# Kernel optimization log

Hardware: AMD Instinct MI355X
Metric: run time of the kernel (lower is better)

The kernel has to match this reference:

```python
import jax, jax.numpy as jnp
import numpy as np

N = 20000      # num clique nodes
E = 320000     # num edges
H = 256        # hidden_channels
OUT = 128      # out_channels
T = 3          # num_timesteps
NEG = 0.01     # GAT negative_slope
NA = 60000     # num atoms (unused arg sizing)


def setup_inputs() -> dict:
    key = jax.random.key(0)
    ks = jax.random.split(key, 12)
    s = 1.0 / np.sqrt(H)
    return {
        "x_clique": jax.random.normal(ks[0], (N, H), jnp.float32),
        "W_gat": jax.random.normal(ks[1], (H, H), jnp.float32) * s,
        "att_src": jax.random.normal(ks[2], (H,), jnp.float32) * s,
        "att_dst": jax.random.normal(ks[3], (H,), jnp.float32) * s,
        "gat_bias": jnp.zeros((H,), jnp.float32),
        "W_ih": jax.random.normal(ks[4], (3 * H, H), jnp.float32) * s,
        "W_hh": jax.random.normal(ks[5], (3 * H, H), jnp.float32) * s,
        "b_ih": jnp.zeros((3 * H,), jnp.float32),
        "b_hh": jnp.zeros((3 * H,), jnp.float32),
        "lin_W": jax.random.normal(ks[6], (OUT, H), jnp.float32) * s,
        "lin_b": jnp.zeros((OUT,), jnp.float32),
        "atom2clique_index": jax.random.randint(ks[7], (2, NA), 0, N, jnp.int64),
        "mol_batch": jax.random.randint(ks[8], (NA,), 0, 32, jnp.int64),
        "clique_batch": jax.random.randint(ks[9], (N,), 0, 32, jnp.int64),
        "clique_edge_index": jax.random.randint(ks[10], (2, E), 0, N, jnp.int64),
    }


def _gat_conv(h, W_gat, att_src, att_dst, gat_bias, src, dst):
    # PyG GATConv, heads=1, no self loops. h: [N,H]
    xp = h @ W_gat.T                                   # [N,H]
    a_e = jax.nn.leaky_relu((xp @ att_src)[src] + (xp @ att_dst)[dst], NEG)  # [E]
    # segment softmax over destination nodes
    m = jax.ops.segment_max(a_e, dst, num_segments=N)  # [N] (-inf for empty)
    e = jnp.exp(a_e - m[dst])                          # [E]
    denom = jax.ops.segment_sum(e, dst, num_segments=N)
    coef = e / jnp.maximum(denom[dst], 1e-16)          # [E]
    out = jax.ops.segment_sum(coef[:, None] * xp[src], dst, num_segments=N)
    return out + gat_bias


def _gru_cell(x, h, W_ih, W_hh, b_ih, b_hh):
    gx = x @ W_ih.T + b_ih                             # [N,3H]
    gh = h @ W_hh.T + b_hh                             # [N,3H]
    xr, xz, xn = jnp.split(gx, 3, axis=-1)
    hr, hz, hn = jnp.split(gh, 3, axis=-1)
    r = jax.nn.sigmoid(xr + hr)
    z = jax.nn.sigmoid(xz + hz)
    n = jnp.tanh(xn + r * hn)
    return (1.0 - z) * n + z * h


def reference(x_clique, W_gat, att_src, att_dst, gat_bias, W_ih, W_hh, b_ih, b_hh,
              lin_W, lin_b, atom2clique_index, mol_batch, clique_batch,
              clique_edge_index):
    src = clique_edge_index[0]
    dst = clique_edge_index[1]
    h = x_clique
    for _ in range(T):  # fixed, small timestep count
        m = _gat_conv(h, W_gat, att_src, att_dst, gat_bias, src, dst)
        m = jax.nn.elu(m)  # dropout p=0.0 -> identity
        h = _gru_cell(m, h, W_ih, W_hh, b_ih, b_hh)
    return h @ lin_W.T + lin_b  # [N, OUT]
```

## Files before the change

kernel.cpp:

```cpp
#include <hip/hip_runtime.h>
#include <math.h>

#define NNODES 20000
#define NROWP  20096
#define NEDGES 320000
#define HDIM   256
#define ODIM   128
#define TSTEPS 3
#define KCAT   512

typedef __bf16 bf16x8 __attribute__((ext_vector_type(8)));
typedef __bf16 bf16x4 __attribute__((ext_vector_type(4)));
typedef float  f32x4  __attribute__((ext_vector_type(4)));

#define LOG2E 1.44269504f
__device__ __forceinline__ float fexp2_(float x){ return __builtin_amdgcn_exp2f(x); }
__device__ __forceinline__ float frcp_(float x){ return __builtin_amdgcn_rcpf(x); }
__device__ __forceinline__ float fsig_(float x){ return frcp_(1.f + fexp2_(-LOG2E*x)); }
__device__ __forceinline__ float ftanh_(float x){ float t = fexp2_(2.f*LOG2E*x); return 1.f - 2.f*frcp_(t+1.f); }
__device__ __forceinline__ float felu_(float x){ return (x>0.f)? x : (fexp2_(LOG2E*x)-1.f); }

__device__ __forceinline__ void load_lds16(const void* g, void* l){
  __builtin_amdgcn_global_load_lds((const __attribute__((address_space(1))) void*)g,
                                   (__attribute__((address_space(3))) void*)l, 16, 0, 0);
}

__device__ __forceinline__ bf16x8 lds_frag64(const __bf16* Ls, int rowbase, int lane, int kk){
  int row = rowbase + (lane&15);
  int g = (lane>>4) + (kk<<2);
  int slot = (row<<3) + (g ^ (row&7));
  return *(const bf16x8*)&Ls[slot<<3];
}

__global__ void setup1_kernel(const int* __restrict__ dst, int* __restrict__ deg,
                              const float* __restrict__ xc, __bf16* __restrict__ Acat,
                              const float* __restrict__ Wih, const float* __restrict__ Whh,
                              const float* __restrict__ Wg, const float* __restrict__ Lw,
                              __bf16* __restrict__ Bf, __bf16* __restrict__ wgb,
                              __bf16* __restrict__ lwb, float* __restrict__ asad){
  int i = blockIdx.x*blockDim.x + threadIdx.x;
  if (i < NEDGES) atomicAdd(&deg[dst[i]], 1);
  if (i < NNODES*64){
    int row = i>>6, c = (i&63)<<2;
    float4 v = *(const float4*)&xc[(size_t)row*HDIM + c];
    bf16x4 o; o[0]=(__bf16)v.x; o[1]=(__bf16)v.y; o[2]=(__bf16)v.z; o[3]=(__bf16)v.w;
    *(bf16x4*)&Acat[(size_t)row*KCAT + 256 + c] = o;
  }
  if (i < 1024*128){
    int row = i>>7, kc = (i&127)<<2;
    int gate = row>>8, c = row&255;
    float4 v = make_float4(0,0,0,0);
    if (gate==0 || gate==1){
      v = (kc<256) ? *(const float4*)&Wih[(size_t)(gate*256+c)*HDIM + kc]
                   : *(const float4*)&Whh[(size_t)(gate*256+c)*HDIM + kc-256];
    } else if (gate==2){
      if (kc<256) v = *(const float4*)&Wih[(size_t)(512+c)*HDIM + kc];
    } else {
      if (kc>=256) v = *(const float4*)&Whh[(size_t)(512+c)*HDIM + kc-256];
    }
    bf16x4 o; o[0]=(__bf16)v.x; o[1]=(__bf16)v.y; o[2]=(__bf16)v.z; o[3]=(__bf16)v.w;
    *(bf16x4*)&Bf[(size_t)row*KCAT + kc] = o;
  } else if (i < 1024*128 + 256*64){
    int j = i - 1024*128;
    float4 v = ((const float4*)Wg)[j];
    bf16x4 o; o[0]=(__bf16)v.x; o[1]=(__bf16)v.y; o[2]=(__bf16)v.z; o[3]=(__bf16)v.w;
    ((bf16x4*)wgb)[j] = o;
  } else if (i < 1024*128 + 256*64 + 128*64){
    int j = i - 1024*128 - 256*64;
    float4 v = ((const float4*)Lw)[j];
    bf16x4 o; o[0]=(__bf16)v.x; o[1]=(__bf16)v.y; o[2]=(__bf16)v.z; o[3]=(__bf16)v.w;
    ((bf16x4*)lwb)[j] = o;
  }
  if (i < 2*NNODES) asad[i] = 0.f;
}

__global__ void scan_kernel(const int* __restrict__ deg, int* __restrict__ rowptr){
  const int PER = 20;
  int tid = threadIdx.x, lane = tid&63, w = tid>>6;
  int base = tid*PER;
  int v[PER]; int s = 0;
  #pragma unroll
  for (int k=0;k<PER;k++){
    v[k] = (base+k < NNODES)? deg[base+k] : 0;
    s += v[k];
  }
  int incl = s;
  #pragma unroll
  for (int off=1; off<64; off<<=1){
    int t = __shfl_up(incl, off);
    if (lane >= off) incl += t;
  }
  __shared__ int wtot[16];
  if (lane==63) wtot[w] = incl;
  __syncthreads();
  if (w==0 && lane<16){
    int x = wtot[lane];
    #pragma unroll
    for (int off=1; off<16; off<<=1){
      int t = __shfl_up(x, off);
      if (lane >= off) x += t;
    }
    wtot[lane] = x;
  }
  __syncthreads();
  int wbase = (w>0)? wtot[w-1] : 0;
  int run = wbase + incl - s;
  #pragma unroll
  for (int k=0;k<PER;k++){
    if (base+k < NNODES) rowptr[base+k] = run;
    run += v[k];
  }
  if (tid==1023) rowptr[NNODES] = wbase + incl;
}

__global__ void scatter_kernel(const int* __restrict__ src, const int* __restrict__ dst,
                               const int* __restrict__ rowptr, int* __restrict__ fill,
                               int* __restrict__ ssrc){
  int e = blockIdx.x*blockDim.x + threadIdx.x;
  if (e < NEDGES){
    int d = dst[e];
    int pos = rowptr[d] + atomicAdd(&fill[d], 1);
    ssrc[pos] = src[e];
  }
}

template<int YC, bool F32OUT, bool ALPHA>
__global__ __launch_bounds__(256,4)
void mfma_gemm_sm(const __bf16* __restrict__ A, int lda,
                  const __bf16* __restrict__ B,
                  const float* __restrict__ bias,
                  __bf16* __restrict__ Cb, float* __restrict__ Cf,
                  int ldc, int Mreal,
                  const float* __restrict__ att_s, const float* __restrict__ att_d,
                  float* __restrict__ as_, float* __restrict__ ad_){
  __shared__ __bf16 As[64*64];
  __shared__ __bf16 Bs[128*64];
  int bid = blockIdx.x;
  int r0 = (bid/YC)*64, c0 = (bid%YC)*128;
  int tx = threadIdx.x, lane = tx&63, w = tx>>6;
  int rbase = (w&1)*32, cbase = (w>>1)*64;
  f32x4 acc[2][4] = {};
  for (int k0=0; k0<HDIM; k0+=64){
    #pragma unroll
    for (int q=0;q<2;q++){
      int idx = q*256 + w*64 + lane;
      int row = idx>>3, kg = (idx&7) ^ (row&7);
      load_lds16(A + (size_t)(r0+row)*lda + k0 + (kg<<3),
                 (char*)As + (q*256 + w*64)*16);
    }
    #pragma unroll
    for (int q=0;q<4;q++){
      int idx = q*256 + w*64 + lane;
      int row = idx>>3, kg = (idx&7) ^ (row&7);
      load_lds16(B + (size_t)(c0+row)*HDIM + k0 + (kg<<3),
                 (char*)Bs + (q*256 + w*64)*16);
    }
    __syncthreads();
    #pragma unroll
    for (int kk=0;kk<2;kk++){
      bf16x8 a[2], bb[4];
      #pragma unroll
      for (int i=0;i<2;i++) a[i] = lds_frag64(As, rbase + i*16, lane, kk);
      #pragma unroll
      for (int j=0;j<4;j++) bb[j] = lds_frag64(Bs, cbase + j*16, lane, kk);
      #pragma unroll
      for (int i=0;i<2;i++)
        #pragma unroll
        for (int j=0;j<4;j++)
          acc[i][j] = __builtin_amdgcn_mfma_f32_16x16x32_bf16(a[i], bb[j], acc[i][j], 0,0,0);
    }
    __syncthreads();
  }
  int grb = r0 + rbase, gcb = c0 + cbase;
  #pragma unroll
  for (int i=0;i<2;i++){
    #pragma unroll
    for (int j=0;j<4;j++){
      int gc = gcb + j*16 + (lane&15);
      float bv = F32OUT ? bias[gc] : 0.f;
      #pragma unroll
      for (int r=0;r<4;r++){
        int gr = grb + i*16 + ((lane>>4)<<2) + r;
        if (gr >= Mreal) continue;
        float v = acc[i][j][r] + bv;
        if (F32OUT) Cf[(size_t)gr*ldc + gc] = v;
        else        Cb[(size_t)gr*ldc + gc] = (__bf16)v;
      }
    }
  }
  if (ALPHA){
    float ps[2][4] = {}, pd[2][4] = {};
    #pragma unroll
    for (int j=0;j<4;j++){
      int gc = gcb + j*16 + (lane&15);
      float sv = att_s[gc], dv = att_d[gc];
      #pragma unroll
      for (int i=0;i<2;i++)
        #pragma unroll
        for (int r=0;r<4;r++){
          ps[i][r] += acc[i][j][r]*sv;
          pd[i][r] += acc[i][j][r]*dv;
        }
    }
    #pragma unroll
    for (int m=1;m<16;m<<=1){
      #pragma unroll
      for (int i=0;i<2;i++)
        #pragma unroll
        for (int r=0;r<4;r++){
          ps[i][r] += __shfl_xor(ps[i][r], m);
          pd[i][r] += __shfl_xor(pd[i][r], m);
        }
    }
    if ((lane&15)==0){
      #pragma unroll
      for (int i=0;i<2;i++)
        #pragma unroll
        for (int r=0;r<4;r++){
          int gr = grb + i*16 + ((lane>>4)<<2) + r;
          if (gr < Mreal){
            atomicAdd(&as_[gr], ps[i][r]);
            atomicAdd(&ad_[gr], pd[i][r]);
          }
        }
    }
  }
}

__global__ __launch_bounds__(256,8)
void gat_aggregate_kernel(const __bf16* __restrict__ xpb, const float* __restrict__ as_,
                          const float* __restrict__ ad_, const int* __restrict__ rowptr,
                          const int* __restrict__ ssrc, const float* __restrict__ gat_bias,
                          __bf16* __restrict__ Acat){
  int node = blockIdx.x*4 + (threadIdx.x>>6);
  int lane = threadIdx.x & 63;
  if (node >= NNODES) return;
  int beg = rowptr[node], end = rowptr[node+1];
  int deg = end - beg;
  float adv = ad_[node];
  int half = lane>>5, col = lane&31;

  float acc[8] = {0,0,0,0,0,0,0,0};

  if (deg <= 64){
    float a = -INFINITY; int sreg = 0;
    if (lane < deg){
      sreg = ssrc[beg+lane];
      a = as_[sreg] + adv;
      a = (a>0.f)? a : 0.01f*a;
    }
    float mx = a;
    #pragma unroll
    for (int off=32; off; off>>=1) mx = fmaxf(mx, __shfl_xor(mx,off));
    float e = (lane<deg)? fexp2_(LOG2E*(a-mx)) : 0.f;
    float sm = e;
    #pragma unroll
    for (int off=32; off; off>>=1) sm += __shfl_xor(sm,off);
    float creg = e*frcp_(fmaxf(sm,1e-16f));

    int j = 0;
    for (; j+16<=deg; j+=16){
      float cc[8]; int rr[8]; bf16x8 vv[8];
      #pragma unroll
      for (int k=0;k<8;k++){
        cc[k] = __shfl(creg, j+2*k+half);
        rr[k] = __shfl(sreg, j+2*k+half);
      }
      #pragma unroll
      for (int k=0;k<8;k++) vv[k] = *(const bf16x8*)&xpb[(size_t)rr[k]*HDIM + col*8];
      #pragma unroll
      for (int k=0;k<8;k++)
        #pragma unroll
        for (int t=0;t<8;t++) acc[t] += cc[k]*(float)vv[k][t];
    }
    for (; j+8<=deg; j+=8){
      float cc[4]; int rr[4]; bf16x8 vv[4];
      #pragma unroll
      for (int k=0;k<4;k++){
        cc[k] = __shfl(creg, j+2*k+half);
        rr[k] = __shfl(sreg, j+2*k+half);
      }
      #pragma unroll
      for (int k=0;k<4;k++) vv[k] = *(const bf16x8*)&xpb[(size_t)rr[k]*HDIM + col*8];
      #pragma unroll
      for (int k=0;k<4;k++)
        #pragma unroll
        for (int t=0;t<8;t++) acc[t] += cc[k]*(float)vv[k][t];
    }
    for (; j+4<=deg; j+=4){
      float c0=__shfl(creg,j+half),  c1=__shfl(creg,j+2+half);
      int   r0=__shfl(sreg,j+half),  r1=__shfl(sreg,j+2+half);
      bf16x8 v0 = *(const bf16x8*)&xpb[(size_t)r0*HDIM + col*8];
      bf16x8 v1 = *(const bf16x8*)&xpb[(size_t)r1*HDIM + col*8];
      #pragma unroll
      for (int t=0;t<8;t++) acc[t] += c0*(float)v0[t] + c1*(float)v1[t];
    }
    for (; j<deg; j+=2){
      int jj = j + half;
      float cf = __shfl(creg, jj);
      int   rw = __shfl(sreg, jj);
      if (jj < deg){
        bf16x8 v = *(const bf16x8*)&xpb[(size_t)rw*HDIM + col*8];
        #pragma unroll
        for (int t=0;t<8;t++) acc[t] += cf*(float)v[t];
      }
    }
  } else {
    float mx = -INFINITY;
    for (int e=beg+lane; e<end; e+=64){
      float a = as_[ssrc[e]] + adv;
      a = (a>0.f)? a : 0.01f*a;
      mx = fmaxf(mx, a);
    }
    #pragma unroll
    for (int off=32; off; off>>=1) mx = fmaxf(mx, __shfl_xor(mx,off));
    float sm = 0.f;
    for (int e=beg+lane; e<end; e+=64){
      float a = as_[ssrc[e]] + adv;
      a = (a>0.f)? a : 0.01f*a;
      sm += fexp2_(LOG2E*(a-mx));
    }
    #pragma unroll
    for (int off=32; off; off>>=1) sm += __shfl_xor(sm,off);
    float rsc = frcp_(fmaxf(sm,1e-16f));
    for (int j=0; j<deg; j+=2){
      int jj = j + half;
      if (jj < deg){
        int rw = ssrc[beg+jj];
        float a = as_[rw] + adv;
        a = (a>0.f)? a : 0.01f*a;
        float cf = fexp2_(LOG2E*(a-mx))*rsc;
        bf16x8 v = *(const bf16x8*)&xpb[(size_t)rw*HDIM + col*8];
        #pragma unroll
        for (int t=0;t<8;t++) acc[t] += cf*(float)v[t];
      }
    }
  }

  #pragma unroll
  for (int t=0;t<8;t++) acc[t] += __shfl_down(acc[t], 32);
  if (half==0){
    float4 b0 = *(const float4*)&gat_bias[col*8];
    float4 b1 = *(const float4*)&gat_bias[col*8+4];
    float bb[8] = {b0.x,b0.y,b0.z,b0.w,b1.x,b1.y,b1.z,b1.w};
    bf16x8 ov;
    #pragma unroll
    for (int t=0;t<8;t++) ov[t] = (__bf16)felu_(acc[t]+bb[t]);
    *(bf16x8*)&Acat[(size_t)node*KCAT + col*8] = ov;
  }
}

__global__ __launch_bounds__(256,4)
void gru_mfma_kernel(const __bf16* __restrict__ Acat, __bf16* __restrict__ AcatN,
                     const __bf16* __restrict__ Bf,
                     const float* __restrict__ bih, const float* __restrict__ bhh,
                     float* __restrict__ as_, float* __restrict__ ad_){
  __shared__ __bf16 As[64*64];
  __shared__ __bf16 Bs[256*64];
  int bid = blockIdx.x;
  int r0 = (bid>>2)*64, c0 = (bid&3)*64;
  int tx = threadIdx.x, lane = tx&63, w = tx>>6;
  int rbase = (w&1)*32, cbase = (w>>1)*32;
  f32x4 acc[4][2][2] = {};
  for (int k0=0; k0<KCAT; k0+=64){
    #pragma unroll
    for (int q=0;q<2;q++){
      int idx = q*256 + w*64 + lane;
      int row = idx>>3, kg = (idx&7) ^ (row&7);
      load_lds16(Acat + (size_t)(r0+row)*KCAT + k0 + (kg<<3),
                 (char*)As + (q*256 + w*64)*16);
    }
    #pragma unroll
    for (int q=0;q<8;q++){
      int idx = q*256 + w*64 + lane;
      int row = idx>>3, kg = (idx&7) ^ (row&7);
      int gate = row>>6, colr = row&63;
      load_lds16(Bf + (size_t)(gate*256 + c0 + colr)*KCAT + k0 + (kg<<3),
                 (char*)Bs + (q*256 + w*64)*16);
    }
    __syncthreads();
    #pragma unroll
    for (int kk=0;kk<2;kk++){
      bf16x8 a[2], bb[4][2];
      #pragma unroll
      for (int i=0;i<2;i++) a[i] = lds_frag64(As, rbase + i*16, lane, kk);
      #pragma unroll
      for (int g=0;g<4;g++)
        #pragma unroll
        for (int j=0;j<2;j++) bb[g][j] = lds_frag64(Bs, g*64 + cbase + j*16, lane, kk);
      #pragma unroll
      for (int g=0;g<4;g++)
        #pragma unroll
        for (int i=0;i<2;i++)
          #pragma unroll
          for (int j=0;j<2;j++)
            acc[g][i][j] = __builtin_amdgcn_mfma_f32_16x16x32_bf16(a[i], bb[g][j], acc[g][i][j], 0,0,0);
    }
    __syncthreads();
  }
  int grb = r0 + rbase;
  #pragma unroll
  for (int i=0;i<2;i++){
    #pragma unroll
    for (int j=0;j<2;j++){
      int gc = c0 + cbase + j*16 + (lane&15);
      float br_ = bih[gc]     + bhh[gc];
      float bz_ = bih[256+gc] + bhh[256+gc];
      float bnx = bih[512+gc];
      float bnh = bhh[512+gc];
      #pragma unroll
      for (int r=0;r<4;r++){
        int gr = grb + i*16 + ((lane>>4)<<2) + r;
        if (gr >= NNODES) continue;
        float hold = (float)Acat[(size_t)gr*KCAT + 256 + gc];
        float rr = fsig_(acc[0][i][j][r] + br_);
        float zz = fsig_(acc[1][i][j][r] + bz_);
        float nn = ftanh_(acc[2][i][j][r] + bnx + rr*(acc[3][i][j][r] + bnh));
        AcatN[(size_t)gr*KCAT + 256 + gc] = (__bf16)((1.f-zz)*nn + zz*hold);
      }
    }
  }
  if ((bid&3)==0 && (w>>1)==0 && (lane&15)==0){
    #pragma unroll
    for (int i=0;i<2;i++)
      #pragma unroll
      for (int r=0;r<4;r++){
        int gr = grb + i*16 + ((lane>>4)<<2) + r;
        if (gr < NNODES){ as_[gr] = 0.f; ad_[gr] = 0.f; }
      }
  }
}

extern "C" void kernel_launch(void* const* d_in, const int* in_sizes, int n_in,
                              void* d_out, int out_size, void* d_ws, size_t ws_size,
                              hipStream_t stream) {
  const float* x_clique = (const float*)d_in[0];
  const float* W_gat    = (const float*)d_in[1];
  const float* att_src  = (const float*)d_in[2];
  const float* att_dst  = (const float*)d_in[3];
  const float* gat_bias = (const float*)d_in[4];
  const float* W_ih     = (const float*)d_in[5];
  const float* W_hh     = (const float*)d_in[6];
  const float* b_ih     = (const float*)d_in[7];
  const float* b_hh     = (const float*)d_in[8];
  const float* lin_W    = (const float*)d_in[9];
  const float* lin_b    = (const float*)d_in[10];
  const int*   eidx     = (const int*)d_in[14];
  float* out = (float*)d_out;

  const int* src = eidx;
  const int* dst = eidx + NEDGES;

  const size_t ACAT = (size_t)NROWP*KCAT;
  __bf16* AcA  = (__bf16*)d_ws;
  __bf16* AcB  = AcA + ACAT;
  __bf16* xpb  = AcB + ACAT;
  __bf16* Bf   = xpb + (size_t)NROWP*HDIM;
  __bf16* wgb  = Bf  + (size_t)1024*KCAT;
  __bf16* lwb  = wgb + (size_t)HDIM*HDIM;
  float* as_   = (float*)(lwb + (size_t)ODIM*HDIM);
  float* ad_   = as_ + NNODES;
  int* deg     = (int*)(ad_ + NNODES);
  int* fill    = deg + NNODES;
  int* rowptr  = fill + NNODES;
  int* ssrc    = rowptr + (NNODES+1);

  hipMemsetAsync(deg, 0, 2*NNODES*sizeof(int), stream);
  setup1_kernel<<<NNODES*64/256, 256, 0, stream>>>(
      dst, deg, x_clique, AcA, W_ih, W_hh, W_gat, lin_W, Bf, wgb, lwb, as_);
  scan_kernel<<<1, 1024, 0, stream>>>(deg, rowptr);
  scatter_kernel<<<(NEDGES+255)/256, 256, 0, stream>>>(src, dst, rowptr, fill, ssrc);

  const int RB64 = NROWP/64;
  __bf16* Ac = AcA;
  __bf16* An = AcB;
  for (int t=0; t<TSTEPS; t++){
    mfma_gemm_sm<2,false,true><<<RB64*2, 256, 0, stream>>>(
        Ac + 256, KCAT, wgb, nullptr, xpb, nullptr, HDIM, NNODES,
        att_src, att_dst, as_, ad_);
    gat_aggregate_kernel<<<(NNODES+3)/4, 256, 0, stream>>>(xpb, as_, ad_, rowptr, ssrc, gat_bias, Ac);
    gru_mfma_kernel<<<RB64*4, 256, 0, stream>>>(Ac, An, Bf, b_ih, b_hh, as_, ad_);
    __bf16* tmp = Ac; Ac = An; An = tmp;
  }
  mfma_gemm_sm<1,true,false><<<RB64, 256, 0, stream>>>(
      Ac + 256, KCAT, lwb, lin_b, nullptr, out, ODIM, NNODES,
      nullptr, nullptr, nullptr, nullptr);
}
```

Measured before the change: 361.2 us.

## Double-buffer LDS in GEMM kernels, retile GRU GEMM, add XCD-aware block swizzle

Both MFMA GEMM kernels now use two LDS buffers, so the global-to-LDS load for the next K slice is issued while the current slice is being multiplied. The aim is to hide load latency behind compute. The GRU kernel is retiled from 64 rows x 64 cols per gate to 128 rows x 32 cols per gate, which changes how often A and B tiles are reused. Block IDs are remapped so that neighbouring tiles land on the same XCD, for better L2 locality. In exchange, LDS use per block roughly doubles and the launch-bounds occupancy hints are lowered, so fewer blocks fit on each CU.

```diff
diff --git a/kernel.cpp b/kernel.cpp
--- a/kernel.cpp
+++ b/kernel.cpp
@@ -30,6 +30,14 @@
   int g = (lane>>4) + (kk<<2);
   int slot = (row<<3) + (g ^ (row&7));
   return *(const bf16x8*)&Ls[slot<<3];
+}
+
+template<int NWG>
+__device__ __forceinline__ int xcd_swz(int b){
+  constexpr int Q = NWG/8, R = NWG%8;
+  int x = b & 7, i = b >> 3;
+  if (R == 0) return x*Q + i;
+  return (x < R) ? (x*(Q+1) + i) : (R*(Q+1) + (x-R)*Q + i);
 }
 
 __global__ void setup1_kernel(const int* __restrict__ dst, int* __restrict__ deg,
@@ -124,8 +132,8 @@
   }
 }
 
-template<int YC, bool F32OUT, bool ALPHA>
-__global__ __launch_bounds__(256,4)
+template<int YC, bool F32OUT, bool ALPHA, int NWG>
+__global__ __launch_bounds__(256,3)
 void mfma_gemm_sm(const __bf16* __restrict__ A, int lda,
                   const __bf16* __restrict__ B,
                   const float* __restrict__ bias,
@@ -133,36 +141,44 @@
                   int ldc, int Mreal,
                   const float* __restrict__ att_s, const float* __restrict__ att_d,
                   float* __restrict__ as_, float* __restrict__ ad_){
-  __shared__ __bf16 As[64*64];
-  __shared__ __bf16 Bs[128*64];
-  int bid = blockIdx.x;
-  int r0 = (bid/YC)*64, c0 = (bid%YC)*128;
+  __shared__ __bf16 As[2][64*64];
+  __shared__ __bf16 Bs[2][128*64];
+  int wgid = xcd_swz<NWG>(blockIdx.x);
+  int r0 = (wgid/YC)*64, c0 = (wgid%YC)*128;
   int tx = threadIdx.x, lane = tx&63, w = tx>>6;
   int rbase = (w&1)*32, cbase = (w>>1)*64;
   f32x4 acc[2][4] = {};
-  for (int k0=0; k0<HDIM; k0+=64){
+
+  auto stage = [&](int k0, int s){
     #pragma unroll
     for (int q=0;q<2;q++){
       int idx = q*256 + w*64 + lane;
       int row = idx>>3, kg = (idx&7) ^ (row&7);
       load_lds16(A + (size_t)(r0+row)*lda + k0 + (kg<<3),
-                 (char*)As + (q*256 + w*64)*16);
+                 (char*)&As[s][0] + (q*256 + w*64)*16);
     }
     #pragma unroll
     for (int q=0;q<4;q++){
       int idx = q*256 + w*64 + lane;
       int row = idx>>3, kg = (idx&7) ^ (row&7);
       load_lds16(B + (size_t)(c0+row)*HDIM + k0 + (kg<<3),
-                 (char*)Bs + (q*256 + w*64)*16);
-    }
-    __syncthreads();
+                 (char*)&Bs[s][0] + (q*256 + w*64)*16);
+    }
+  };
+
+  stage(0, 0);
+  __syncthreads();
+  #pragma unroll
+  for (int t=0; t<HDIM/64; t++){
+    const int cur = t & 1;
+    if (t+1 < HDIM/64) stage((t+1)*64, cur^1);
     #pragma unroll
     for (int kk=0;kk<2;kk++){
       bf16x8 a[2], bb[4];
       #pragma unroll
-      for (int i=0;i<2;i++) a[i] = lds_frag64(As, rbase + i*16, lane, kk);
-      #pragma unroll
-      for (int j=0;j<4;j++) bb[j] = lds_frag64(Bs, cbase + j*16, lane, kk);
+      for (int i=0;i<2;i++) a[i] = lds_frag64(&As[cur][0], rbase + i*16, lane, kk);
+      #pragma unroll
+      for (int j=0;j<4;j++) bb[j] = lds_frag64(&Bs[cur][0], cbase + j*16, lane, kk);
       #pragma unroll
       for (int i=0;i<2;i++)
         #pragma unroll
@@ -350,44 +366,53 @@
   }
 }
 
-__global__ __launch_bounds__(256,4)
+#define RB128 (NROWP/128)
+__global__ __launch_bounds__(256,2)
 void gru_mfma_kernel(const __bf16* __restrict__ Acat, __bf16* __restrict__ AcatN,
                      const __bf16* __restrict__ Bf,
                      const float* __restrict__ bih, const float* __restrict__ bhh,
                      float* __restrict__ as_, float* __restrict__ ad_){
-  __shared__ __bf16 As[64*64];
-  __shared__ __bf16 Bs[256*64];
-  int bid = blockIdx.x;
-  int r0 = (bid>>2)*64, c0 = (bid&3)*64;
+  __shared__ __bf16 As[2][128*64];
+  __shared__ __bf16 Bs[2][128*64];
+  int wgid = xcd_swz<RB128*8>(blockIdx.x);
+  int r0 = (wgid>>3)*128, c0 = (wgid&7)*32;
   int tx = threadIdx.x, lane = tx&63, w = tx>>6;
-  int rbase = (w&1)*32, cbase = (w>>1)*32;
+  int rbase = w*32;
   f32x4 acc[4][2][2] = {};
-  for (int k0=0; k0<KCAT; k0+=64){
-    #pragma unroll
-    for (int q=0;q<2;q++){
+
+  auto stage = [&](int k0, int s){
+    #pragma unroll
+    for (int q=0;q<4;q++){
       int idx = q*256 + w*64 + lane;
       int row = idx>>3, kg = (idx&7) ^ (row&7);
       load_lds16(Acat + (size_t)(r0+row)*KCAT + k0 + (kg<<3),
-                 (char*)As + (q*256 + w*64)*16);
-    }
-    #pragma unroll
-    for (int q=0;q<8;q++){
+                 (char*)&As[s][0] + (q*256 + w*64)*16);
+    }
+    #pragma unroll
+    for (int q=0;q<4;q++){
       int idx = q*256 + w*64 + lane;
       int row = idx>>3, kg = (idx&7) ^ (row&7);
-      int gate = row>>6, colr = row&63;
+      int gate = row>>5, colr = row&31;
       load_lds16(Bf + (size_t)(gate*256 + c0 + colr)*KCAT + k0 + (kg<<3),
-                 (char*)Bs + (q*256 + w*64)*16);
-    }
-    __syncthreads();
+                 (char*)&Bs[s][0] + (q*256 + w*64)*16);
+    }
+  };
+
+  stage(0, 0);
+  __syncthreads();
+  #pragma unroll
+  for (int t=0; t<KCAT/64; t++){
+    const int cur = t & 1;
+    if (t+1 < KCAT/64) stage((t+1)*64, cur^1);
     #pragma unroll
     for (int kk=0;kk<2;kk++){
       bf16x8 a[2], bb[4][2];
       #pragma unroll
-      for (int i=0;i<2;i++) a[i] = lds_frag64(As, rbase + i*16, lane, kk);
+      for (int i=0;i<2;i++) a[i] = lds_frag64(&As[cur][0], rbase + i*16, lane, kk);
       #pragma unroll
       for (int g=0;g<4;g++)
         #pragma unroll
-        for (int j=0;j<2;j++) bb[g][j] = lds_frag64(Bs, g*64 + cbase + j*16, lane, kk);
+        for (int j=0;j<2;j++) bb[g][j] = lds_frag64(&Bs[cur][0], g*32 + j*16, lane, kk);
       #pragma unroll
       for (int g=0;g<4;g++)
         #pragma unroll
@@ -403,7 +428,7 @@
   for (int i=0;i<2;i++){
     #pragma unroll
     for (int j=0;j<2;j++){
-      int gc = c0 + cbase + j*16 + (lane&15);
+      int gc = c0 + j*16 + (lane&15);
       float br_ = bih[gc]     + bhh[gc];
       float bz_ = bih[256+gc] + bhh[256+gc];
       float bnx = bih[512+gc];
@@ -420,7 +445,7 @@
       }
     }
   }
-  if ((bid&3)==0 && (w>>1)==0 && (lane&15)==0){
+  if ((wgid&7)==0 && (lane&15)==0){
     #pragma unroll
     for (int i=0;i<2;i++)
       #pragma unroll
@@ -475,14 +500,14 @@
   __bf16* Ac = AcA;
   __bf16* An = AcB;
   for (int t=0; t<TSTEPS; t++){
-    mfma_gemm_sm<2,false,true><<<RB64*2, 256, 0, stream>>>(
+    mfma_gemm_sm<2,false,true,(NROWP/64)*2><<<RB64*2, 256, 0, stream>>>(
         Ac + 256, KCAT, wgb, nullptr, xpb, nullptr, HDIM, NNODES,
         att_src, att_dst, as_, ad_);
     gat_aggregate_kernel<<<(NNODES+3)/4, 256, 0, stream>>>(xpb, as_, ad_, rowptr, ssrc, gat_bias, Ac);
-    gru_mfma_kernel<<<RB64*4, 256, 0, stream>>>(Ac, An, Bf, b_ih, b_hh, as_, ad_);
+    gru_mfma_kernel<<<RB128*8, 256, 0, stream>>>(Ac, An, Bf, b_ih, b_hh, as_, ad_);
     __bf16* tmp = Ac; Ac = An; An = tmp;
   }
-  mfma_gemm_sm<1,true,false><<<RB64, 256, 0, stream>>>(
+  mfma_gemm_sm<1,true,false,NROWP/64><<<RB64, 256, 0, stream>>>(
       Ac + 256, KCAT, lwb, lin_b, nullptr, out, ODIM, NNODES,
       nullptr, nullptr, nullptr, nullptr);
 }
```

Result: no change. 368.3 us (+2.0%).
